# Performance work log

Measured on AMD Instinct MI355X. Metric: run time of the kernel, lower is better.

Reference implementation:

```python
import jax, jax.numpy as jnp
import numpy as np

DIM = 1024
NUM_EXPERTS = 8
N_TOKENS = 8192


def setup_inputs() -> dict:
    key = jax.random.key(0)
    ks = jax.random.split(key, 6)
    z_real = jax.random.normal(ks[0], (N_TOKENS, DIM), dtype=jnp.float32)
    z_imag = jax.random.normal(ks[1], (N_TOKENS, DIM), dtype=jnp.float32)
    # gate: nn.Linear(2*dim, E) -> weight [E, 2*dim], bias [E]
    Wg = jax.random.normal(ks[2], (NUM_EXPERTS, 2 * DIM), dtype=jnp.float32) * (1.0 / np.sqrt(2 * DIM))
    bg = jnp.zeros((NUM_EXPERTS,), dtype=jnp.float32)
    # experts: per-expert real/imag square weights [E, dim, dim] (nn.Linear layout: [out, in])
    Wr = jax.random.normal(ks[3], (NUM_EXPERTS, DIM, DIM), dtype=jnp.float32) * (1.0 / np.sqrt(DIM))
    Wi = jax.random.normal(ks[4], (NUM_EXPERTS, DIM, DIM), dtype=jnp.float32) * (1.0 / np.sqrt(DIM))
    return {"z_real": z_real, "z_imag": z_imag, "Wg": Wg, "bg": bg, "Wr": Wr, "Wi": Wi}


def reference(z_real, z_imag, Wg, bg, Wr, Wi):
    # gate over concat(real, imag)
    z_flat = jnp.concatenate([z_real, z_imag], axis=-1)            # [N, 2D]
    gates = jax.nn.softmax(z_flat @ Wg.T + bg, axis=-1)            # [N, E]
    # all-expert complex linear: y = x @ W^T with W [E, out, in]
    rr = jnp.einsum('ni,eoi->neo', z_real, Wr)                     # real @ Wr
    ii = jnp.einsum('ni,eoi->neo', z_imag, Wi)                     # imag @ Wi
    ri = jnp.einsum('ni,eoi->neo', z_imag, Wr)                     # imag @ Wr
    ir = jnp.einsum('ni,eoi->neo', z_real, Wi)                     # real @ Wi
    out_r = jnp.einsum('ne,neo->no', gates, rr - ii)               # [N, D]
    out_i = jnp.einsum('ne,neo->no', gates, ri + ir)               # [N, D]
    return jnp.stack([out_r, out_i], axis=0)                       # [2, N, D]
```

## Files before the change

kernel.cpp:

```cpp
#include <hip/hip_runtime.h>
#include <hip/hip_bf16.h>

#define NTOK 8192
#define DIM 1024
#define NEXP 8
#define NT 256
#define BK 64

typedef float f32x4 __attribute__((ext_vector_type(4)));
typedef short s16x8 __attribute__((ext_vector_type(8)));
typedef unsigned short u16;
typedef unsigned short u16x4 __attribute__((ext_vector_type(4)));

__device__ __forceinline__ u16 f2bf(float f) {
    __hip_bfloat16 h = __float2bfloat16(f);
    return *reinterpret_cast<u16*>(&h);
}
__device__ __forceinline__ float bf2f(u16 u) {
    unsigned v = ((unsigned)u) << 16;
    return __uint_as_float(v);
}

#define GLOAD16(gsrc, ldst)                                                     \
    __builtin_amdgcn_global_load_lds(                                           \
        (const __attribute__((address_space(1))) void*)(gsrc),                  \
        (__attribute__((address_space(3))) void*)(ldst), 16, 0, 0)

#define MFMA16(a, b, c) __builtin_amdgcn_mfma_f32_16x16x32_bf16((a), (b), (c), 0, 0, 0)
#define SGB() __builtin_amdgcn_sched_barrier(0)

__global__ __launch_bounds__(256) void gates_kernel(
    const float* __restrict__ zr, const float* __restrict__ zi,
    const float* __restrict__ Wg, const float* __restrict__ bg,
    float* __restrict__ gates)
{
    const int wave = threadIdx.x >> 6, lane = threadIdx.x & 63;
    const int n = blockIdx.x * 4 + wave;

    float v[32];
    const float* zrp = zr + (size_t)n * DIM;
    const float* zip = zi + (size_t)n * DIM;
#pragma unroll
    for (int j = 0; j < 16; ++j) v[j] = zrp[j * 64 + lane];
#pragma unroll
    for (int j = 0; j < 16; ++j) v[16 + j] = zip[j * 64 + lane];

    float s[NEXP];
#pragma unroll
    for (int e = 0; e < NEXP; ++e) {
        const float* wrow = Wg + (size_t)e * (2 * DIM);
        float a = 0.f;
#pragma unroll
        for (int j = 0; j < 32; ++j) a += v[j] * wrow[j * 64 + lane];
#pragma unroll
        for (int m = 32; m; m >>= 1) a += __shfl_xor(a, m);
        s[e] = a + bg[e];
    }
    float mx = s[0];
#pragma unroll
    for (int e = 1; e < NEXP; ++e) mx = fmaxf(mx, s[e]);
    float p[NEXP], sum = 0.f;
#pragma unroll
    for (int e = 0; e < NEXP; ++e) { p[e] = expf(s[e] - mx); sum += p[e]; }
    const float inv = 1.f / sum;
    if (lane == 0) {
#pragma unroll
        for (int e = 0; e < NEXP; ++e) gates[(size_t)n * NEXP + e] = p[e] * inv;
    }
}

__global__ __launch_bounds__(256) void cvt4_kernel(
    const float* __restrict__ zr, const float* __restrict__ zi,
    const float* __restrict__ Wr, const float* __restrict__ Wi,
    u16* __restrict__ zr16, u16* __restrict__ zi16,
    u16* __restrict__ Wr16, u16* __restrict__ Wi16)
{
    const size_t total = (size_t)NEXP * DIM * DIM / 4;
    for (size_t i = (size_t)blockIdx.x * 256 + threadIdx.x; i < total;
         i += (size_t)gridDim.x * 256) {
        f32x4 a = ((const f32x4*)zr)[i];
        f32x4 b = ((const f32x4*)zi)[i];
        f32x4 c = ((const f32x4*)Wr)[i];
        f32x4 d = ((const f32x4*)Wi)[i];
        u16x4 pa, pb, pc, pd;
#pragma unroll
        for (int j = 0; j < 4; ++j) {
            pa[j] = f2bf(a[j]); pb[j] = f2bf(b[j]);
            pc[j] = f2bf(c[j]); pd[j] = f2bf(d[j]);
        }
        ((u16x4*)zr16)[i] = pa;
        ((u16x4*)zi16)[i] = pb;
        ((u16x4*)Wr16)[i] = pc;
        ((u16x4*)Wi16)[i] = pd;
    }
}

__global__ __launch_bounds__(512, 2) void moe_gemm13(
    const u16* __restrict__ zr16, const u16* __restrict__ zi16,
    const u16* __restrict__ Wr16, const u16* __restrict__ Wi16,
    const float* __restrict__ gates, float* __restrict__ out)
{
    extern __shared__ u16 lds[];

    const int linear = blockIdx.x + 32 * (blockIdx.y + 4 * blockIdx.z);
    const int xcd = linear & 7;
    const int bm = xcd * 4 + ((linear >> 3) & 3);
    const int grp2 = linear >> 5;
    const int bn = grp2 & 3;
    const int sel = grp2 >> 2;

    const int tid = threadIdx.x;
    const int lane = tid & 63;
    const int wid = tid >> 6;
    const int wr = wid >> 2;
    const int wc = wid & 3;

    const int srow = tid >> 3;
    const int schunk = (tid & 7) ^ (srow & 7);
    int arow[4], gidx[4], brow[4];
#pragma unroll
    for (int j = 0; j < 4; ++j) {
        const int gr = bm * 256 + srow + j * 64;
        arow[j] = gr * DIM + schunk * 8;
        gidx[j] = gr * NEXP;
        brow[j] = (bn * 256 + srow + j * 64) * DIM + schunk * 8;
    }

    const int cg = lane >> 4;
    const int l7 = lane & 7;
    const int ach0 = (cg ^ l7) * 8;
    const int ach1 = ((4 + cg) ^ l7) * 8;
    const int arbase = (wr * 128 + (lane & 15)) * BK;
    const int brbase = (wc * 64 + (lane & 15)) * BK;

    f32x4 acc[8][4];
#pragma unroll
    for (int m = 0; m < 8; ++m)
#pragma unroll
        for (int n = 0; n < 4; ++n) acc[m][n] = (f32x4){0.f, 0.f, 0.f, 0.f};

    const u16* Asrc = sel ? zi16 : zr16;
    const u16* Bseg = Wr16;
    float sg[4];
#pragma unroll
    for (int j = 0; j < 4; ++j) sg[j] = gates[gidx[j]];

    {
        s16x8 ga0[4];
#pragma unroll
        for (int j = 0; j < 4; ++j) ga0[j] = *(const s16x8*)(Asrc + arow[j]);
#pragma unroll
        for (int q = 0; q < 4; ++q)
            GLOAD16(Bseg + brow[q], &lds[32768 + (q * 512 + tid) * 8]);
#pragma unroll
        for (int j = 0; j < 4; ++j) {
            s16x8 w;
#pragma unroll
            for (int e = 0; e < 8; ++e)
                w[e] = (short)f2bf(bf2f((u16)ga0[j][e]) * sg[j]);
            *(s16x8*)&lds[(tid + j * 512) * 8] = w;
        }
        asm volatile("s_waitcnt vmcnt(0) lgkmcnt(0)" ::: "memory");
        __builtin_amdgcn_s_barrier();
    }

    int buf = 0;
#pragma unroll 1
    for (int t = 0; t < NT; ++t) {
        const int t1 = t + 1;
        if ((t1 & 15) == 0) {
            const int seg = t1 >> 4;
            const int e = (seg >> 1) & 7;
            const int half = seg & 1;
            Asrc = (half ^ sel) ? zi16 : zr16;
            Bseg = (half ? Wi16 : Wr16) + (size_t)e * DIM * DIM;
            const float sgn = (sel == 0 && half == 1) ? -1.f : 1.f;
#pragma unroll
            for (int j = 0; j < 4; ++j) sg[j] = sgn * gates[gidx[j] + e];
        }
        const int ka = (t1 & 15) << 6;
        const int ab = buf * 16384 + arbase;
        const int bb = 32768 + buf * 16384 + brbase;
        const int sa = (buf ^ 1) * 16384;
        const int sb = 32768 + (buf ^ 1) * 16384;

        s16x8 ga[4];
#pragma unroll
        for (int j = 0; j < 4; ++j) ga[j] = *(const s16x8*)(Asrc + arow[j] + ka);
        GLOAD16(Bseg + brow[0] + ka, &lds[sb + (0 * 512 + tid) * 8]);
        GLOAD16(Bseg + brow[1] + ka, &lds[sb + (1 * 512 + tid) * 8]);
        GLOAD16(Bseg + brow[2] + ka, &lds[sb + (2 * 512 + tid) * 8]);
        GLOAD16(Bseg + brow[3] + ka, &lds[sb + (3 * 512 + tid) * 8]);

        s16x8 b0[4], a01[8];
#pragma unroll
        for (int n = 0; n < 4; ++n) b0[n] = *(const s16x8*)&lds[bb + n * 1024 + ach0];
#pragma unroll
        for (int m = 0; m < 8; ++m) a01[m] = *(const s16x8*)&lds[ab + m * 1024 + ach0];
        asm volatile("s_waitcnt lgkmcnt(8)" ::: "memory");
        SGB();
        __builtin_amdgcn_s_barrier();
        asm volatile("s_waitcnt lgkmcnt(0)" ::: "memory");
        SGB();
        __builtin_amdgcn_s_setprio(1);
#pragma unroll
        for (int m = 0; m < 8; ++m)
#pragma unroll
            for (int n = 0; n < 4; ++n) acc[m][n] = MFMA16(a01[m], b0[n], acc[m][n]);
        __builtin_amdgcn_s_setprio(0);
        SGB();
        __builtin_amdgcn_s_barrier();

        s16x8 b1[4], a23[8];
#pragma unroll
        for (int n = 0; n < 4; ++n) b1[n] = *(const s16x8*)&lds[bb + n * 1024 + ach1];
#pragma unroll
        for (int m = 0; m < 8; ++m) a23[m] = *(const s16x8*)&lds[ab + m * 1024 + ach1];
#pragma unroll
        for (int j = 0; j < 4; ++j) {
            s16x8 w;
#pragma unroll
            for (int e = 0; e < 8; ++e)
                w[e] = (short)f2bf(bf2f((u16)ga[j][e]) * sg[j]);
            *(s16x8*)&lds[sa + (tid + j * 512) * 8] = w;
        }
        asm volatile("s_waitcnt lgkmcnt(8)" ::: "memory");
        SGB();
        __builtin_amdgcn_s_barrier();
        asm volatile("s_waitcnt lgkmcnt(0)" ::: "memory");
        SGB();
        __builtin_amdgcn_s_setprio(1);
#pragma unroll
        for (int m = 0; m < 8; ++m)
#pragma unroll
            for (int n = 0; n < 4; ++n) acc[m][n] = MFMA16(a23[m], b1[n], acc[m][n]);
        __builtin_amdgcn_s_setprio(0);
        asm volatile("s_waitcnt vmcnt(0)" ::: "memory");
        SGB();
        __builtin_amdgcn_s_barrier();

        buf ^= 1;
    }

    float* op = out + (size_t)sel * NTOK * DIM;
    const int col0 = bn * 256 + wc * 64 + (lane & 15);
    const int row0 = bm * 256 + wr * 128 + ((lane >> 4) << 2);
#pragma unroll
    for (int m = 0; m < 8; ++m)
#pragma unroll
        for (int n = 0; n < 4; ++n)
#pragma unroll
            for (int j = 0; j < 4; ++j)
                op[(size_t)(row0 + m * 16 + j) * DIM + col0 + n * 16] = acc[m][n][j];
}

extern "C" void kernel_launch(void* const* d_in, const int* in_sizes, int n_in,
                              void* d_out, int out_size, void* d_ws, size_t ws_size,
                              hipStream_t stream) {
    const float* zr = (const float*)d_in[0];
    const float* zi = (const float*)d_in[1];
    const float* Wg = (const float*)d_in[2];
    const float* bg = (const float*)d_in[3];
    const float* Wr = (const float*)d_in[4];
    const float* Wi = (const float*)d_in[5];
    float* out = (float*)d_out;

    const size_t NELEM = (size_t)NEXP * DIM * DIM;
    u16* zr16 = (u16*)d_ws;
    u16* zi16 = zr16 + NELEM;
    u16* Wr16 = zi16 + NELEM;
    u16* Wi16 = Wr16 + NELEM;
    float* gates = (float*)(Wi16 + NELEM);

    cvt4_kernel<<<2048, 256, 0, stream>>>(zr, zi, Wr, Wi, zr16, zi16, Wr16, Wi16);
    gates_kernel<<<NTOK / 4, 256, 0, stream>>>(zr, zi, Wg, bg, gates);

    hipFuncSetAttribute((const void*)moe_gemm13,
                        hipFuncAttributeMaxDynamicSharedMemorySize, 131072);
    dim3 grid(NTOK / 256, DIM / 256, 2);
    moe_gemm13<<<grid, 512, 131072, stream>>>(zr16, zi16, Wr16, Wi16, gates, out);
}
```

Measured before the change: 574.3 us.

## Apply gates to fp32 accumulators per segment instead of scaling A tiles

The GEMM no longer rescales A by the gate and restages it through LDS. It now loads unscaled bf16 A fragments straight from global memory into registers and accumulates each expert/half segment separately, then folds that segment into a running total weighted by the gate in fp32. Gates are stored transposed so each lane can read four consecutive rows' gates as one vector. Block tiles shrink from 256x256 to 128x256 with a 512-block 1D grid, LDS use is halved, and there is one barrier per K step instead of two. In exchange, A is read directly from global memory with no LDS reuse, a second accumulator set raises register pressure, and the gate multiply is more precise than before.

```diff
diff --git a/kernel.cpp b/kernel.cpp
--- a/kernel.cpp
+++ b/kernel.cpp
@@ -6,6 +6,7 @@
 #define NEXP 8
 #define NT 256
 #define BK 64
+#define NELEMZ ((size_t)NTOK * DIM)
 
 typedef float f32x4 __attribute__((ext_vector_type(4)));
 typedef short s16x8 __attribute__((ext_vector_type(8)));
@@ -16,10 +17,6 @@
     __hip_bfloat16 h = __float2bfloat16(f);
     return *reinterpret_cast<u16*>(&h);
 }
-__device__ __forceinline__ float bf2f(u16 u) {
-    unsigned v = ((unsigned)u) << 16;
-    return __uint_as_float(v);
-}
 
 #define GLOAD16(gsrc, ldst)                                                     \
     __builtin_amdgcn_global_load_lds(                                           \
@@ -27,12 +24,11 @@
         (__attribute__((address_space(3))) void*)(ldst), 16, 0, 0)
 
 #define MFMA16(a, b, c) __builtin_amdgcn_mfma_f32_16x16x32_bf16((a), (b), (c), 0, 0, 0)
-#define SGB() __builtin_amdgcn_sched_barrier(0)
 
 __global__ __launch_bounds__(256) void gates_kernel(
     const float* __restrict__ zr, const float* __restrict__ zi,
     const float* __restrict__ Wg, const float* __restrict__ bg,
-    float* __restrict__ gates)
+    float* __restrict__ gT)
 {
     const int wave = threadIdx.x >> 6, lane = threadIdx.x & 63;
     const int n = blockIdx.x * 4 + wave;
@@ -65,7 +61,7 @@
     const float inv = 1.f / sum;
     if (lane == 0) {
 #pragma unroll
-        for (int e = 0; e < NEXP; ++e) gates[(size_t)n * NEXP + e] = p[e] * inv;
+        for (int e = 0; e < NEXP; ++e) gT[(size_t)e * NTOK + n] = p[e] * inv;
     }
 }
 
@@ -75,7 +71,7 @@
     u16* __restrict__ zr16, u16* __restrict__ zi16,
     u16* __restrict__ Wr16, u16* __restrict__ Wi16)
 {
-    const size_t total = (size_t)NEXP * DIM * DIM / 4;
+    const size_t total = NELEMZ / 4;
     for (size_t i = (size_t)blockIdx.x * 256 + threadIdx.x; i < total;
          i += (size_t)gridDim.x * 256) {
         f32x4 a = ((const f32x4*)zr)[i];
@@ -95,19 +91,19 @@
     }
 }
 
-__global__ __launch_bounds__(512, 2) void moe_gemm13(
+__global__ __launch_bounds__(512, 2) void moe_gemm15(
     const u16* __restrict__ zr16, const u16* __restrict__ zi16,
     const u16* __restrict__ Wr16, const u16* __restrict__ Wi16,
-    const float* __restrict__ gates, float* __restrict__ out)
+    const float* __restrict__ gT, float* __restrict__ out)
 {
     extern __shared__ u16 lds[];
 
-    const int linear = blockIdx.x + 32 * (blockIdx.y + 4 * blockIdx.z);
-    const int xcd = linear & 7;
-    const int bm = xcd * 4 + ((linear >> 3) & 3);
-    const int grp2 = linear >> 5;
-    const int bn = grp2 & 3;
-    const int sel = grp2 >> 2;
+    const int bid = blockIdx.x;
+    const int xcd = bid & 7;
+    const int loc = bid >> 3;
+    const int grp = loc & 7;
+    const int bm = xcd * 8 + (loc >> 3);
+    const int bn = grp & 3, sel = grp >> 2;
 
     const int tid = threadIdx.x;
     const int lane = tid & 63;
@@ -117,141 +113,129 @@
 
     const int srow = tid >> 3;
     const int schunk = (tid & 7) ^ (srow & 7);
-    int arow[4], gidx[4], brow[4];
-#pragma unroll
-    for (int j = 0; j < 4; ++j) {
-        const int gr = bm * 256 + srow + j * 64;
-        arow[j] = gr * DIM + schunk * 8;
-        gidx[j] = gr * NEXP;
+    int brow[4];
+#pragma unroll
+    for (int j = 0; j < 4; ++j)
         brow[j] = (bn * 256 + srow + j * 64) * DIM + schunk * 8;
-    }
 
     const int cg = lane >> 4;
     const int l7 = lane & 7;
     const int ach0 = (cg ^ l7) * 8;
     const int ach1 = ((4 + cg) ^ l7) * 8;
-    const int arbase = (wr * 128 + (lane & 15)) * BK;
     const int brbase = (wc * 64 + (lane & 15)) * BK;
 
-    f32x4 acc[8][4];
-#pragma unroll
-    for (int m = 0; m < 8; ++m)
-#pragma unroll
-        for (int n = 0; n < 4; ++n) acc[m][n] = (f32x4){0.f, 0.f, 0.f, 0.f};
+    const int arowb = (bm * 128 + wr * 64 + (lane & 15)) * DIM + (lane >> 4) * 8;
+
+    const int grow0 = bm * 128 + wr * 64 + ((lane >> 4) << 2);
+
+    f32x4 acc[4][4], tot[4][4];
+#pragma unroll
+    for (int m = 0; m < 4; ++m)
+#pragma unroll
+        for (int n = 0; n < 4; ++n) {
+            acc[m][n] = (f32x4){0.f, 0.f, 0.f, 0.f};
+            tot[m][n] = (f32x4){0.f, 0.f, 0.f, 0.f};
+        }
 
     const u16* Asrc = sel ? zi16 : zr16;
-    const u16* Bseg = Wr16;
-    float sg[4];
-#pragma unroll
-    for (int j = 0; j < 4; ++j) sg[j] = gates[gidx[j]];
-
-    {
-        s16x8 ga0[4];
-#pragma unroll
-        for (int j = 0; j < 4; ++j) ga0[j] = *(const s16x8*)(Asrc + arow[j]);
-#pragma unroll
-        for (int q = 0; q < 4; ++q)
-            GLOAD16(Bseg + brow[q], &lds[32768 + (q * 512 + tid) * 8]);
-#pragma unroll
-        for (int j = 0; j < 4; ++j) {
-            s16x8 w;
-#pragma unroll
-            for (int e = 0; e < 8; ++e)
-                w[e] = (short)f2bf(bf2f((u16)ga0[j][e]) * sg[j]);
-            *(s16x8*)&lds[(tid + j * 512) * 8] = w;
-        }
-        asm volatile("s_waitcnt vmcnt(0) lgkmcnt(0)" ::: "memory");
-        __builtin_amdgcn_s_barrier();
-    }
-
-    int buf = 0;
+    const u16* Bseg1 = Wr16;
+    f32x4 sgm[4];
+
+#pragma unroll
+    for (int q = 0; q < 4; ++q)
+        GLOAD16(Wr16 + brow[q], &lds[(q * 512 + tid) * 8]);
+    asm volatile("s_waitcnt vmcnt(0)" ::: "memory");
+    __builtin_amdgcn_s_barrier();
+
 #pragma unroll 1
     for (int t = 0; t < NT; ++t) {
+        if ((t & 15) == 0) {
+            const int seg = t >> 4;
+            if (t) {
+#pragma unroll
+                for (int m = 0; m < 4; ++m)
+#pragma unroll
+                    for (int n = 0; n < 4; ++n) {
+#pragma unroll
+                        for (int j = 0; j < 4; ++j)
+                            tot[m][n][j] += sgm[m][j] * acc[m][n][j];
+                        acc[m][n] = (f32x4){0.f, 0.f, 0.f, 0.f};
+                    }
+            }
+            const int e = seg >> 1, half = seg & 1;
+            Asrc = (half ^ sel) ? zi16 : zr16;
+            const float sgn = (sel == 0 && half == 1) ? -1.f : 1.f;
+#pragma unroll
+            for (int m = 0; m < 4; ++m) {
+                const f32x4 g = *(const f32x4*)&gT[(size_t)e * NTOK + grow0 + m * 16];
+#pragma unroll
+                for (int j = 0; j < 4; ++j) sgm[m][j] = sgn * g[j];
+            }
+        }
         const int t1 = t + 1;
         if ((t1 & 15) == 0) {
             const int seg = t1 >> 4;
             const int e = (seg >> 1) & 7;
-            const int half = seg & 1;
-            Asrc = (half ^ sel) ? zi16 : zr16;
-            Bseg = (half ? Wi16 : Wr16) + (size_t)e * DIM * DIM;
-            const float sgn = (sel == 0 && half == 1) ? -1.f : 1.f;
-#pragma unroll
-            for (int j = 0; j < 4; ++j) sg[j] = sgn * gates[gidx[j] + e];
-        }
-        const int ka = (t1 & 15) << 6;
-        const int ab = buf * 16384 + arbase;
-        const int bb = 32768 + buf * 16384 + brbase;
-        const int sa = (buf ^ 1) * 16384;
-        const int sb = 32768 + (buf ^ 1) * 16384;
-
-        s16x8 ga[4];
-#pragma unroll
-        for (int j = 0; j < 4; ++j) ga[j] = *(const s16x8*)(Asrc + arow[j] + ka);
-        GLOAD16(Bseg + brow[0] + ka, &lds[sb + (0 * 512 + tid) * 8]);
-        GLOAD16(Bseg + brow[1] + ka, &lds[sb + (1 * 512 + tid) * 8]);
-        GLOAD16(Bseg + brow[2] + ka, &lds[sb + (2 * 512 + tid) * 8]);
-        GLOAD16(Bseg + brow[3] + ka, &lds[sb + (3 * 512 + tid) * 8]);
-
-        s16x8 b0[4], a01[8];
+            Bseg1 = ((seg & 1) ? Wi16 : Wr16) + (size_t)e * DIM * DIM;
+        }
+        const int kb = (t & 15) << 6;
+        const int kb1 = (t1 & 15) << 6;
+        const int rs = t & 1;
+        const int bb = rs * 16384 + brbase;
+        const int sb = (rs ^ 1) * 16384;
+
+        GLOAD16(Bseg1 + brow[0] + kb1, &lds[sb + (0 * 512 + tid) * 8]);
+        GLOAD16(Bseg1 + brow[1] + kb1, &lds[sb + (1 * 512 + tid) * 8]);
+        GLOAD16(Bseg1 + brow[2] + kb1, &lds[sb + (2 * 512 + tid) * 8]);
+        GLOAD16(Bseg1 + brow[3] + kb1, &lds[sb + (3 * 512 + tid) * 8]);
+        s16x8 a[8];
+#pragma unroll
+        for (int ks = 0; ks < 2; ++ks)
+#pragma unroll
+            for (int m = 0; m < 4; ++m)
+                a[ks * 4 + m] = *(const s16x8*)(Asrc + arowb + m * 16 * DIM + ks * 32 + kb);
+
+        s16x8 b0[4];
 #pragma unroll
         for (int n = 0; n < 4; ++n) b0[n] = *(const s16x8*)&lds[bb + n * 1024 + ach0];
-#pragma unroll
-        for (int m = 0; m < 8; ++m) a01[m] = *(const s16x8*)&lds[ab + m * 1024 + ach0];
-        asm volatile("s_waitcnt lgkmcnt(8)" ::: "memory");
-        SGB();
+        __builtin_amdgcn_s_setprio(1);
+#pragma unroll
+        for (int m = 0; m < 4; ++m)
+#pragma unroll
+            for (int n = 0; n < 4; ++n) acc[m][n] = MFMA16(a[m], b0[n], acc[m][n]);
+        __builtin_amdgcn_s_setprio(0);
+
+        s16x8 b1[4];
+#pragma unroll
+        for (int n = 0; n < 4; ++n) b1[n] = *(const s16x8*)&lds[bb + n * 1024 + ach1];
+        __builtin_amdgcn_s_setprio(1);
+#pragma unroll
+        for (int m = 0; m < 4; ++m)
+#pragma unroll
+            for (int n = 0; n < 4; ++n) acc[m][n] = MFMA16(a[4 + m], b1[n], acc[m][n]);
+        __builtin_amdgcn_s_setprio(0);
+
+        asm volatile("s_waitcnt vmcnt(0) lgkmcnt(0)" ::: "memory");
         __builtin_amdgcn_s_barrier();
-        asm volatile("s_waitcnt lgkmcnt(0)" ::: "memory");
-        SGB();
-        __builtin_amdgcn_s_setprio(1);
-#pragma unroll
-        for (int m = 0; m < 8; ++m)
-#pragma unroll
-            for (int n = 0; n < 4; ++n) acc[m][n] = MFMA16(a01[m], b0[n], acc[m][n]);
-        __builtin_amdgcn_s_setprio(0);
-        SGB();
-        __builtin_amdgcn_s_barrier();
-
-        s16x8 b1[4], a23[8];
-#pragma unroll
-        for (int n = 0; n < 4; ++n) b1[n] = *(const s16x8*)&lds[bb + n * 1024 + ach1];
-#pragma unroll
-        for (int m = 0; m < 8; ++m) a23[m] = *(const s16x8*)&lds[ab + m * 1024 + ach1];
-#pragma unroll
-        for (int j = 0; j < 4; ++j) {
-            s16x8 w;
-#pragma unroll
-            for (int e = 0; e < 8; ++e)
-                w[e] = (short)f2bf(bf2f((u16)ga[j][e]) * sg[j]);
-            *(s16x8*)&lds[sa + (tid + j * 512) * 8] = w;
-        }
-        asm volatile("s_waitcnt lgkmcnt(8)" ::: "memory");
-        SGB();
-        __builtin_amdgcn_s_barrier();
-        asm volatile("s_waitcnt lgkmcnt(0)" ::: "memory");
-        SGB();
-        __builtin_amdgcn_s_setprio(1);
-#pragma unroll
-        for (int m = 0; m < 8; ++m)
-#pragma unroll
-            for (int n = 0; n < 4; ++n) acc[m][n] = MFMA16(a23[m], b1[n], acc[m][n]);
-        __builtin_amdgcn_s_setprio(0);
-        asm volatile("s_waitcnt vmcnt(0)" ::: "memory");
-        SGB();
-        __builtin_amdgcn_s_barrier();
-
-        buf ^= 1;
-    }
+    }
+
+#pragma unroll
+    for (int m = 0; m < 4; ++m)
+#pragma unroll
+        for (int n = 0; n < 4; ++n)
+#pragma unroll
+            for (int j = 0; j < 4; ++j)
+                tot[m][n][j] += sgm[m][j] * acc[m][n][j];
 
     float* op = out + (size_t)sel * NTOK * DIM;
     const int col0 = bn * 256 + wc * 64 + (lane & 15);
-    const int row0 = bm * 256 + wr * 128 + ((lane >> 4) << 2);
-#pragma unroll
-    for (int m = 0; m < 8; ++m)
+#pragma unroll
+    for (int m = 0; m < 4; ++m)
 #pragma unroll
         for (int n = 0; n < 4; ++n)
 #pragma unroll
             for (int j = 0; j < 4; ++j)
-                op[(size_t)(row0 + m * 16 + j) * DIM + col0 + n * 16] = acc[m][n][j];
+                op[(size_t)(grow0 + m * 16 + j) * DIM + col0 + n * 16] = tot[m][n][j];
 }
 
 extern "C" void kernel_launch(void* const* d_in, const int* in_sizes, int n_in,
@@ -265,18 +249,16 @@
     const float* Wi = (const float*)d_in[5];
     float* out = (float*)d_out;
 
-    const size_t NELEM = (size_t)NEXP * DIM * DIM;
     u16* zr16 = (u16*)d_ws;
-    u16* zi16 = zr16 + NELEM;
-    u16* Wr16 = zi16 + NELEM;
-    u16* Wi16 = Wr16 + NELEM;
-    float* gates = (float*)(Wi16 + NELEM);
+    u16* zi16 = zr16 + NELEMZ;
+    u16* Wr16 = zi16 + NELEMZ;
+    u16* Wi16 = Wr16 + NELEMZ;
+    float* gT = (float*)(Wi16 + NELEMZ);
 
     cvt4_kernel<<<2048, 256, 0, stream>>>(zr, zi, Wr, Wi, zr16, zi16, Wr16, Wi16);
-    gates_kernel<<<NTOK / 4, 256, 0, stream>>>(zr, zi, Wg, bg, gates);
-
-    hipFuncSetAttribute((const void*)moe_gemm13,
-                        hipFuncAttributeMaxDynamicSharedMemorySize, 131072);
-    dim3 grid(NTOK / 256, DIM / 256, 2);
-    moe_gemm13<<<grid, 512, 131072, stream>>>(zr16, zi16, Wr16, Wi16, gates, out);
-}
+    gates_kernel<<<NTOK / 4, 256, 0, stream>>>(zr, zi, Wg, bg, gT);
+
+    hipFuncSetAttribute((const void*)moe_gemm15,
+                        hipFuncAttributeMaxDynamicSharedMemorySize, 65536);
+    moe_gemm15<<<512, 512, 65536, stream>>>(zr16, zi16, Wr16, Wi16, gT, out);
+}
```

After: 1.429 ms. 149% more time.
